# Optimization experiments

Hardware: AMD Instinct MI355X
Metric: run time of the kernel (lower is better)

## Reference

```python
import jax, jax.numpy as jnp
import numpy as np

EMBED_DIM = 1024
NUM_HEADS = 16
D_K = EMBED_DIM // NUM_HEADS


def setup_inputs() -> dict:
    key = jax.random.key(0)
    kx, kq, kk, kv, ko = jax.random.split(key, 5)
    scale = 1.0 / np.sqrt(EMBED_DIM)
    return {
        "x": jax.random.normal(kx, (4, 2048, EMBED_DIM), dtype=jnp.float32),
        # nn.Linear weights are [out, in]; we store them the same way.
        "w_q": jax.random.normal(kq, (EMBED_DIM, EMBED_DIM), dtype=jnp.float32) * scale,
        "w_k": jax.random.normal(kk, (EMBED_DIM, EMBED_DIM), dtype=jnp.float32) * scale,
        "w_v": jax.random.normal(kv, (EMBED_DIM, EMBED_DIM), dtype=jnp.float32) * scale,
        "w_o": jax.random.normal(ko, (EMBED_DIM, EMBED_DIM), dtype=jnp.float32) * scale,
    }


def reference(x, w_q, w_k, w_v, w_o):
    B, S, E = x.shape
    H, Dk = NUM_HEADS, D_K

    def proj(w):  # [B,S,E] @ [E,E]^T -> [B,H,S,Dk]
        y = jnp.einsum('bse,fe->bsf', x, w)
        return y.reshape(B, S, H, Dk).transpose(0, 2, 1, 3)

    q, k, v = proj(w_q), proj(w_k), proj(w_v)
    scores = jnp.einsum('bhsd,bhtd->bhst', q, k) / jnp.sqrt(jnp.float32(Dk))
    attn = jax.nn.softmax(scores, axis=-1)  # dropout p=0 -> identity
    out = jnp.einsum('bhst,bhtd->bhsd', attn, v)
    out = out.transpose(0, 2, 1, 3).reshape(B, S, E)
    return jnp.einsum('bse,fe->bsf', out, w_o)
```

## Files before the change

### kernel.cpp

```cpp
#include <hip/hip_runtime.h>
#include <stdint.h>

typedef unsigned short u16;
typedef __attribute__((ext_vector_type(8))) short bf16x8;
typedef __attribute__((ext_vector_type(4))) float f32x4;
typedef __attribute__((ext_vector_type(16))) float f32x16;

#define EMB 1024
#define SLEN 2048
#define NHD 16
#define DKH 64

__device__ __forceinline__ u16 f2bf(float f) {
  uint32_t u = __float_as_uint(f);
  u = (u + 0x7fffu + ((u >> 16) & 1u)) >> 16;
  return (u16)u;
}

__device__ __forceinline__ void load_lds16(const void* g, void* l) {
  __builtin_amdgcn_global_load_lds(
      (const __attribute__((address_space(1))) uint32_t*)g,
      (__attribute__((address_space(3))) uint32_t*)l, 16, 0, 0);
}

__global__ __launch_bounds__(256) void cvt_f32_bf16(const float* __restrict__ in,
                                                    u16* __restrict__ out, int n4) {
  int i = blockIdx.x * 256 + threadIdx.x;
  if (i >= n4) return;
  float4 v = ((const float4*)in)[i];
  union { u16 h[4]; uint64_t q; } o;
  o.h[0] = f2bf(v.x); o.h[1] = f2bf(v.y); o.h[2] = f2bf(v.z); o.h[3] = f2bf(v.w);
  ((uint64_t*)out)[i] = o.q;
}

__global__ __launch_bounds__(256) void cvt_w4(
    const float* __restrict__ w0, const float* __restrict__ w1,
    const float* __restrict__ w2, const float* __restrict__ w3,
    u16* __restrict__ o0, u16* __restrict__ o1,
    u16* __restrict__ o2, u16* __restrict__ o3) {
  const float* in = (blockIdx.y == 0) ? w0 : (blockIdx.y == 1) ? w1
                    : (blockIdx.y == 2) ? w2 : w3;
  u16* out = (blockIdx.y == 0) ? o0 : (blockIdx.y == 1) ? o1
             : (blockIdx.y == 2) ? o2 : o3;
  int i = blockIdx.x * 256 + threadIdx.x;
  float4 v = ((const float4*)in)[i];
  union { u16 h[4]; uint64_t q; } o;
  o.h[0] = f2bf(v.x); o.h[1] = f2bf(v.y); o.h[2] = f2bf(v.z); o.h[3] = f2bf(v.w);
  ((uint64_t*)out)[i] = o.q;
}

template<int MODE>
__device__ __forceinline__ void gemm_body(const u16* __restrict__ A,
                                          const u16* __restrict__ W,
                                          void* __restrict__ C) {
  __shared__ __align__(16) u16 At[128 * 32];
  __shared__ __align__(16) u16 Bt[128 * 32];
  const int tid = threadIdx.x;
  const int l = tid & 63, w = tid >> 6;
  const int wm = w >> 1, wn = w & 1;
  const int bm = blockIdx.y * 128, bn = blockIdx.x * 128;
  const int lr = l & 15, lg = l >> 4;

  f32x4 acc[4][4] = {};

  const int e0 = w * 1024 + l * 8;
  const int r0 = e0 >> 5, c0 = e0 & 31;
  const int e1 = e0 + 512;
  const int r1 = e1 >> 5, c1 = e1 & 31;
  const u16* Ag0 = A + (size_t)(bm + r0) * EMB + c0;
  const u16* Ag1 = A + (size_t)(bm + r1) * EMB + c1;
  const u16* Wg0 = W + (size_t)(bn + r0) * EMB + c0;
  const u16* Wg1 = W + (size_t)(bn + r1) * EMB + c1;
  u16* Al = At + w * 1024;
  u16* Bl = Bt + w * 1024;

  for (int k0 = 0; k0 < EMB; k0 += 32) {
    load_lds16(Ag0 + k0, Al);
    load_lds16(Ag1 + k0, Al + 512);
    load_lds16(Wg0 + k0, Bl);
    load_lds16(Wg1 + k0, Bl + 512);
    asm volatile("s_waitcnt vmcnt(0)" ::: "memory");
    __syncthreads();
    bf16x8 af[4], bf[4];
#pragma unroll
    for (int i = 0; i < 4; ++i)
      af[i] = *(const bf16x8*)(At + (wm * 64 + i * 16 + lr) * 32 + lg * 8);
#pragma unroll
    for (int j = 0; j < 4; ++j)
      bf[j] = *(const bf16x8*)(Bt + (wn * 64 + j * 16 + lr) * 32 + lg * 8);
#pragma unroll
    for (int i = 0; i < 4; ++i)
#pragma unroll
      for (int j = 0; j < 4; ++j)
        acc[i][j] = __builtin_amdgcn_mfma_f32_16x16x32_bf16(af[i], bf[j], acc[i][j], 0, 0, 0);
    __syncthreads();
  }

  if (MODE == 2) {
#pragma unroll
    for (int i = 0; i < 4; ++i) {
      const int m0 = bm + wm * 64 + i * 16 + lg * 4;
      const int bb = m0 >> 11;
      const int ss = m0 & 2047;
#pragma unroll
      for (int j = 0; j < 4; ++j) {
        const int n = bn + wn * 64 + j * 16 + lr;
        const int hh = n >> 6, dd = n & 63;
        union { u16 h[4]; uint64_t q; } pk;
#pragma unroll
        for (int r = 0; r < 4; ++r) pk.h[r] = f2bf(acc[i][j][r]);
        *(uint64_t*)((u16*)C + ((size_t)((bb * 16 + hh) * 64 + dd)) * 2048 + ss) = pk.q;
      }
    }
  } else {
#pragma unroll
    for (int i = 0; i < 4; ++i) {
      const int mb = bm + wm * 64 + i * 16 + lg * 4;
#pragma unroll
      for (int j = 0; j < 4; ++j) {
        const int col = bn + wn * 64 + j * 16 + lr;
#pragma unroll
        for (int r = 0; r < 4; ++r) {
          float v = acc[i][j][r];
          if (MODE == 1) v *= 0.18033688011112042f;
          if (MODE == 3)
            ((float*)C)[(size_t)(mb + r) * EMB + col] = v;
          else
            ((u16*)C)[(size_t)(mb + r) * EMB + col] = f2bf(v);
        }
      }
    }
  }
}

__global__ __launch_bounds__(256) void gemm_qkv(
    const u16* __restrict__ A,
    const u16* __restrict__ wq, const u16* __restrict__ wk, const u16* __restrict__ wv,
    u16* __restrict__ Qo, u16* __restrict__ Ko, u16* __restrict__ Vo) {
  if (blockIdx.z == 0) gemm_body<1>(A, wq, Qo);
  else if (blockIdx.z == 1) gemm_body<0>(A, wk, Ko);
  else gemm_body<2>(A, wv, Vo);
}

__global__ __launch_bounds__(256) void gemm_out(const u16* __restrict__ A,
                                                const u16* __restrict__ W,
                                                float* __restrict__ C) {
  gemm_body<3>(A, W, C);
}

__global__ __launch_bounds__(512, 4) void attn_fwd(const u16* __restrict__ Q,
                                                   const u16* __restrict__ K,
                                                   const u16* __restrict__ VT,
                                                   u16* __restrict__ O) {
  __shared__ __align__(16) u16 lds[3][2][64 * 64];
  const int tid = threadIdx.x;
  const int l = tid & 63, w = tid >> 6;
  const int ql = l & 31, hi = l >> 5;
  const int bid = blockIdx.x;
  const int bh = (bid & 7) * 8 + (bid >> 6);
  const int qt = (bid >> 3) & 7;
  const int b = bh >> 4, h = bh & 15;
  const int qw = qt * 256 + w * 32;
  const size_t qkb = ((size_t)b * SLEN) * EMB + h * DKH;
  const size_t vb = (size_t)bh * DKH * SLEN;

  const int srow = tid >> 3;
  const int scb = ((tid & 7) * 16) ^ ((srow & 7) << 4);
  const u16* Ksrc = K + qkb + (size_t)srow * EMB + (scb >> 1);
  const u16* Vsrc = VT + vb + (size_t)srow * SLEN + (scb >> 1);

  auto stage = [&](int buf, int t) {
    load_lds16(Ksrc + (size_t)t * 64 * EMB, (char*)(&lds[buf][0][0]) + w * 1024);
    load_lds16(Vsrc + t * 64, (char*)(&lds[buf][1][0]) + w * 1024);
  };

  bf16x8 qf[4];
#pragma unroll
  for (int ks = 0; ks < 4; ++ks)
    qf[ks] = *(const bf16x8*)(Q + qkb + (size_t)(qw + ql) * EMB + ks * 16 + hi * 8);

  f32x16 accd[2] = {};
  float lsum = 0.f;

  stage(0, 0);
  stage(1, 1);
  int cur = 0;
#pragma unroll 1
  for (int t = 0; t < 32; ++t) {
    if (t < 30) {
      int nb = cur + 2; if (nb >= 3) nb -= 3;
      stage(nb, t + 2);
      asm volatile("s_waitcnt vmcnt(4)" ::: "memory");
    } else if (t == 30) {
      asm volatile("s_waitcnt vmcnt(2)" ::: "memory");
    } else {
      asm volatile("s_waitcnt vmcnt(0)" ::: "memory");
    }
    __builtin_amdgcn_s_barrier();

    const u16* Kt = &lds[cur][0][0];
    const u16* Vt = &lds[cur][1][0];

    f32x16 sacc[2] = {};
    __builtin_amdgcn_s_setprio(1);
#pragma unroll
    for (int kf2 = 0; kf2 < 2; ++kf2) {
      const int row = kf2 * 32 + ql;
      const int swz = (row & 7) << 4;
#pragma unroll
      for (int ks = 0; ks < 4; ++ks) {
        bf16x8 kf = *(const bf16x8*)((const char*)Kt + row * 128 +
                                     ((ks * 32 + hi * 16) ^ swz));
        sacc[kf2] = __builtin_amdgcn_mfma_f32_32x32x16_bf16(kf, qf[ks], sacc[kf2], 0, 0, 0);
      }
    }
    __builtin_amdgcn_s_setprio(0);

#pragma unroll
    for (int kf2 = 0; kf2 < 2; ++kf2)
#pragma unroll
      for (int r = 0; r < 16; ++r)
        sacc[kf2][r] = __builtin_amdgcn_exp2f(sacc[kf2][r]);
    float ps[8];
#pragma unroll
    for (int g = 0; g < 8; ++g) {
      const int kf2 = g >> 2, r0 = (g & 3) * 4;
      ps[g] = (sacc[kf2][r0] + sacc[kf2][r0 + 1]) + (sacc[kf2][r0 + 2] + sacc[kf2][r0 + 3]);
    }
    lsum += ((ps[0] + ps[1]) + (ps[2] + ps[3])) + ((ps[4] + ps[5]) + (ps[6] + ps[7]));

    __builtin_amdgcn_s_setprio(1);
#pragma unroll
    for (int ks = 0; ks < 4; ++ks) {
      const int kf2 = ks >> 1;
      const int e0 = (ks & 1) * 8;
      uint32_t a0, a1, b0, b1;
      asm("v_cvt_pk_bf16_f32 %0, %1, %2" : "=v"(a0) : "v"(sacc[kf2][e0 + 0]), "v"(sacc[kf2][e0 + 1]));
      asm("v_cvt_pk_bf16_f32 %0, %1, %2" : "=v"(a1) : "v"(sacc[kf2][e0 + 2]), "v"(sacc[kf2][e0 + 3]));
      asm("v_cvt_pk_bf16_f32 %0, %1, %2" : "=v"(b0) : "v"(sacc[kf2][e0 + 4]), "v"(sacc[kf2][e0 + 5]));
      asm("v_cvt_pk_bf16_f32 %0, %1, %2" : "=v"(b1) : "v"(sacc[kf2][e0 + 6]), "v"(sacc[kf2][e0 + 7]));
      asm("v_permlane32_swap_b32 %0, %1" : "+v"(a0), "+v"(b0));
      asm("v_permlane32_swap_b32 %0, %1" : "+v"(a1), "+v"(b1));
      union { uint32_t d[4]; bf16x8 v; } pa;
      pa.d[0] = a0; pa.d[1] = a1; pa.d[2] = b0; pa.d[3] = b1;
#pragma unroll
      for (int df = 0; df < 2; ++df) {
        const int vr = df * 32 + ql;
        bf16x8 vf = *(const bf16x8*)((const char*)Vt + vr * 128 +
                                     ((ks * 32 + hi * 16) ^ ((vr & 7) << 4)));
        accd[df] = __builtin_amdgcn_mfma_f32_32x32x16_bf16(pa.v, vf, accd[df], 0, 0, 0);
      }
    }
    __builtin_amdgcn_s_setprio(0);
    __builtin_amdgcn_s_barrier();
    ++cur; if (cur == 3) cur = 0;
  }

  lsum += __shfl_xor(lsum, 32, 64);

  __syncthreads();
  u16* slice = &lds[0][0][0] + w * 2048;
#pragma unroll
  for (int reg = 0; reg < 16; ++reg) {
    const int rowq = (reg & 3) + 8 * (reg >> 2) + 4 * hi;
    const float li = 1.0f / __shfl(lsum, rowq, 64);
    slice[rowq * 64 + ql] = f2bf(accd[0][reg] * li);
    slice[rowq * 64 + 32 + ql] = f2bf(accd[1][reg] * li);
  }
  asm volatile("s_waitcnt lgkmcnt(0)" ::: "memory");
#pragma unroll
  for (int j = 0; j < 4; ++j) {
    const int byteoff = j * 1024 + l * 16;
    const int row = byteoff >> 7;
    const int colB = byteoff & 127;
    bf16x8 vv = *(const bf16x8*)((const char*)slice + byteoff);
    *(bf16x8*)(O + qkb + (size_t)(qw + row) * EMB + (colB >> 1)) = vv;
  }
}

extern "C" void kernel_launch(void* const* d_in, const int* in_sizes, int n_in,
                              void* d_out, int out_size, void* d_ws, size_t ws_size,
                              hipStream_t stream) {
  const float* x  = (const float*)d_in[0];
  const float* wq = (const float*)d_in[1];
  const float* wk = (const float*)d_in[2];
  const float* wv = (const float*)d_in[3];
  const float* wo = (const float*)d_in[4];

  char* ws = (char*)d_ws;
  u16* xb  = (u16*)(ws + 0);
  u16* wqb = (u16*)(ws + 16777216);
  u16* wkb = (u16*)(ws + 18874368);
  u16* wvb = (u16*)(ws + 20971520);
  u16* wob = (u16*)(ws + 23068672);
  u16* Qb  = (u16*)(ws + 25165824);
  u16* Kb  = (u16*)(ws + 41943040);
  u16* VTb = (u16*)(ws + 58720256);
  u16* AO  = (u16*)(ws + 75497472);

  cvt_f32_bf16<<<2097152 / 256, 256, 0, stream>>>(x, xb, 2097152);
  cvt_w4<<<dim3(262144 / 256, 4), 256, 0, stream>>>(wq, wk, wv, wo, wqb, wkb, wvb, wob);

  gemm_qkv<<<dim3(8, 64, 3), 256, 0, stream>>>(xb, wqb, wkb, wvb, Qb, Kb, VTb);
  attn_fwd<<<dim3(512), 512, 0, stream>>>(Qb, Kb, VTb, AO);
  gemm_out<<<dim3(8, 64), 256, 0, stream>>>(AO, wob, (float*)d_out);
}
```

Measured before the change: 183.9 us.

## Double-buffer GEMM LDS tiles and remap workgroups across XCDs

The GEMM main loop now double-buffers the A/W tiles in LDS, issuing the next k-slice's global-to-LDS loads before computing on the current slice, so load latency overlaps MFMA work and one barrier per iteration is removed. Both GEMM kernels switch to a 1D grid with a block-id remap ((bid&7)*N + bid>>3) so that consecutive tiles land on the same XCD, which is meant to improve L2 reuse of shared A/W rows. The cost is double the LDS footprint per block, which may lower occupancy.

```diff
diff --git a/kernel.cpp b/kernel.cpp
--- a/kernel.cpp
+++ b/kernel.cpp
@@ -52,13 +52,13 @@
 template<int MODE>
 __device__ __forceinline__ void gemm_body(const u16* __restrict__ A,
                                           const u16* __restrict__ W,
-                                          void* __restrict__ C) {
-  __shared__ __align__(16) u16 At[128 * 32];
-  __shared__ __align__(16) u16 Bt[128 * 32];
+                                          void* __restrict__ C,
+                                          int bm, int bn) {
+  __shared__ __align__(16) u16 At[2][128 * 32];
+  __shared__ __align__(16) u16 Bt[2][128 * 32];
   const int tid = threadIdx.x;
   const int l = tid & 63, w = tid >> 6;
   const int wm = w >> 1, wn = w & 1;
-  const int bm = blockIdx.y * 128, bn = blockIdx.x * 128;
   const int lr = l & 15, lg = l >> 4;
 
   f32x4 acc[4][4] = {};
@@ -71,29 +71,36 @@
   const u16* Ag1 = A + (size_t)(bm + r1) * EMB + c1;
   const u16* Wg0 = W + (size_t)(bn + r0) * EMB + c0;
   const u16* Wg1 = W + (size_t)(bn + r1) * EMB + c1;
-  u16* Al = At + w * 1024;
-  u16* Bl = Bt + w * 1024;
+
+  auto stage = [&](int buf, int k0) {
+    load_lds16(Ag0 + k0, &At[buf][w * 1024]);
+    load_lds16(Ag1 + k0, &At[buf][w * 1024 + 512]);
+    load_lds16(Wg0 + k0, &Bt[buf][w * 1024]);
+    load_lds16(Wg1 + k0, &Bt[buf][w * 1024 + 512]);
+  };
+
+  stage(0, 0);
+  asm volatile("s_waitcnt vmcnt(0)" ::: "memory");
+  __syncthreads();
+  int cur = 0;
 
   for (int k0 = 0; k0 < EMB; k0 += 32) {
-    load_lds16(Ag0 + k0, Al);
-    load_lds16(Ag1 + k0, Al + 512);
-    load_lds16(Wg0 + k0, Bl);
-    load_lds16(Wg1 + k0, Bl + 512);
+    if (k0 + 32 < EMB) stage(cur ^ 1, k0 + 32);
+    bf16x8 af[4], bf[4];
+#pragma unroll
+    for (int i = 0; i < 4; ++i)
+      af[i] = *(const bf16x8*)(&At[cur][(wm * 64 + i * 16 + lr) * 32 + lg * 8]);
+#pragma unroll
+    for (int j = 0; j < 4; ++j)
+      bf[j] = *(const bf16x8*)(&Bt[cur][(wn * 64 + j * 16 + lr) * 32 + lg * 8]);
+#pragma unroll
+    for (int i = 0; i < 4; ++i)
+#pragma unroll
+      for (int j = 0; j < 4; ++j)
+        acc[i][j] = __builtin_amdgcn_mfma_f32_16x16x32_bf16(af[i], bf[j], acc[i][j], 0, 0, 0);
     asm volatile("s_waitcnt vmcnt(0)" ::: "memory");
     __syncthreads();
-    bf16x8 af[4], bf[4];
-#pragma unroll
-    for (int i = 0; i < 4; ++i)
-      af[i] = *(const bf16x8*)(At + (wm * 64 + i * 16 + lr) * 32 + lg * 8);
-#pragma unroll
-    for (int j = 0; j < 4; ++j)
-      bf[j] = *(const bf16x8*)(Bt + (wn * 64 + j * 16 + lr) * 32 + lg * 8);
-#pragma unroll
-    for (int i = 0; i < 4; ++i)
-#pragma unroll
-      for (int j = 0; j < 4; ++j)
-        acc[i][j] = __builtin_amdgcn_mfma_f32_16x16x32_bf16(af[i], bf[j], acc[i][j], 0, 0, 0);
-    __syncthreads();
+    cur ^= 1;
   }
 
   if (MODE == 2) {
@@ -137,15 +144,23 @@
     const u16* __restrict__ A,
     const u16* __restrict__ wq, const u16* __restrict__ wk, const u16* __restrict__ wv,
     u16* __restrict__ Qo, u16* __restrict__ Ko, u16* __restrict__ Vo) {
-  if (blockIdx.z == 0) gemm_body<1>(A, wq, Qo);
-  else if (blockIdx.z == 1) gemm_body<0>(A, wk, Ko);
-  else gemm_body<2>(A, wv, Vo);
+  const int bid = blockIdx.x;
+  const int wgid = (bid & 7) * 192 + (bid >> 3);
+  const int z = wgid >> 9;
+  const int rem = wgid & 511;
+  const int bm = (rem >> 3) * 128, bn = (rem & 7) * 128;
+  if (z == 0) gemm_body<1>(A, wq, Qo, bm, bn);
+  else if (z == 1) gemm_body<0>(A, wk, Ko, bm, bn);
+  else gemm_body<2>(A, wv, Vo, bm, bn);
 }
 
 __global__ __launch_bounds__(256) void gemm_out(const u16* __restrict__ A,
                                                 const u16* __restrict__ W,
                                                 float* __restrict__ C) {
-  gemm_body<3>(A, W, C);
+  const int bid = blockIdx.x;
+  const int wgid = (bid & 7) * 64 + (bid >> 3);
+  const int bm = (wgid >> 3) * 128, bn = (wgid & 7) * 128;
+  gemm_body<3>(A, W, C, bm, bn);
 }
 
 __global__ __launch_bounds__(512, 4) void attn_fwd(const u16* __restrict__ Q,
@@ -301,7 +316,7 @@
   cvt_f32_bf16<<<2097152 / 256, 256, 0, stream>>>(x, xb, 2097152);
   cvt_w4<<<dim3(262144 / 256, 4), 256, 0, stream>>>(wq, wk, wv, wo, wqb, wkb, wvb, wob);
 
-  gemm_qkv<<<dim3(8, 64, 3), 256, 0, stream>>>(xb, wqb, wkb, wvb, Qb, Kb, VTb);
+  gemm_qkv<<<dim3(1536), 256, 0, stream>>>(xb, wqb, wkb, wvb, Qb, Kb, VTb);
   attn_fwd<<<dim3(512), 512, 0, stream>>>(Qb, Kb, VTb, AO);
-  gemm_out<<<dim3(8, 64), 256, 0, stream>>>(AO, wob, (float*)d_out);
-}
+  gemm_out<<<dim3(512), 256, 0, stream>>>(AO, wob, (float*)d_out);
+}
```

Result: slower. 240.4 us (+30.7%).
